# Kernel optimization log

Measured on AMD Instinct MI355X. Metric: run time of the kernel, lower is better.

## Reference

```python
import jax, jax.numpy as jnp
import numpy as np

B, S, D, H, DK, L, DFF, V = 64, 128, 512, 8, 64, 6, 2048, 72
AH = 2          # heads of the internal mask-generating attention encoder (hard-coded n_heads=2)
PRECET = 0.2    # fraction of lowest-attention prefix tokens to mask
NEG = -1e9


def pos_enc(s, d):
    pos = jnp.arange(s, dtype=jnp.float32)[:, None]
    div = jnp.exp(jnp.arange(0, d, 2, dtype=jnp.float32) * (-np.log(10000.0) / d))
    pe = jnp.zeros((s, d), jnp.float32)
    pe = pe.at[:, 0::2].set(jnp.sin(pos * div))
    pe = pe.at[:, 1::2].set(jnp.cos(pos * div))
    return pe


def ln(x, eps=1e-5):  # LayerNorm with default (identity) affine params, as in the source
    m = x.mean(-1, keepdims=True)
    v = ((x - m) ** 2).mean(-1, keepdims=True)
    return (x - m) / jnp.sqrt(v + eps)


def attn_block(x, pad, WQ, WK, WV, WO, heads):
    b, s, _ = x.shape
    dk = WQ.shape[1] // heads
    q = (x @ WQ).reshape(b, s, heads, dk).transpose(0, 2, 1, 3)
    k = (x @ WK).reshape(b, s, heads, dk).transpose(0, 2, 1, 3)
    v = (x @ WV).reshape(b, s, heads, dk).transpose(0, 2, 1, 3)
    scores = jnp.einsum('bhqd,bhkd->bhqk', q, k) / np.sqrt(dk)
    scores = jnp.where(pad[:, None, None, :], NEG, scores)
    attn = jax.nn.softmax(scores, axis=-1)
    ascore = attn.sum(axis=2)                                   # [b, h, s] column sums
    ctx = jnp.einsum('bhqk,bhkd->bqhd', attn, v).reshape(b, s, heads * dk)
    return ln(ctx @ WO + x), attn, ascore


def ffn_block(x, W1, W2):
    return ln(jax.nn.relu(x @ W1) @ W2 + x)


def encode(x, pad, tWQ, tWK, tWV, tFC, tF1, tF2):
    def step(h, p):
        WQ, WK, WV, WO, W1, W2 = p
        h, _, asc = attn_block(h, pad, WQ, WK, WV, WO, H)
        h = ffn_block(h, W1, W2)
        return h, asc.sum(axis=1)                               # sum over heads -> [b, s]
    h, scores = jax.lax.scan(step, x, (tWQ, tWK, tWV, tFC, tF1, tF2))
    return h, scores                                            # scores: [L, b, s]


def creat_mask(col, tokens):
    # col[i, j] == 0 exactly iff token j is pad (softmax of -1e9 underflows to 0).
    b, s = tokens.shape
    iszero = col == 0.0
    has = iszero.any(axis=1)
    j0 = jnp.where(has, jnp.argmax(iszero, axis=1), s)          # first pad position
    kk = jnp.where(has, jnp.ceil(PRECET * j0.astype(jnp.float32)).astype(jnp.int32), 0)
    idx = jnp.arange(s)
    vals = jnp.where(idx[None, :] < j0[:, None], col, jnp.inf)
    ranks = jnp.argsort(jnp.argsort(vals, axis=1), axis=1)      # rank 0 = smallest attention
    keep = (ranks >= kk[:, None]).astype(tokens.dtype)
    return tokens * keep


def pre_head(x, pW1, pb1, pW2, pb2, pW3, pb3):
    x = jax.nn.relu(x @ pW1 + pb1)
    x = jax.nn.relu(x @ pW2 + pb2)
    return x @ pW3 + pb3


def setup_inputs():
    key = jax.random.key(0)
    ks = jax.random.split(key, 18)
    g = lambda k, shp: jax.random.normal(k, shp, jnp.float32) * 0.02
    return {
        'tokens': jax.random.randint(ks[0], (B, S), 0, V, dtype=jnp.int32),
        'emb': g(ks[1], (V, D)),
        'aWQ': g(ks[2], (D, AH * DK)), 'aWK': g(ks[3], (D, AH * DK)), 'aWV': g(ks[4], (D, AH * DK)),
        'aFC': g(ks[5], (AH * DK, D)), 'aF1': g(ks[6], (D, DFF)), 'aF2': g(ks[7], (DFF, D)),
        'tWQ': g(ks[8], (L, D, H * DK)), 'tWK': g(ks[9], (L, D, H * DK)), 'tWV': g(ks[10], (L, D, H * DK)),
        'tFC': g(ks[11], (L, H * DK, D)), 'tF1': g(ks[12], (L, D, DFF)), 'tF2': g(ks[13], (L, DFF, D)),
        'pW1': g(ks[14], (D * S, 1024)), 'pb1': jnp.zeros((1024,), jnp.float32),
        'pW2': g(ks[15], (1024, 512)), 'pb2': jnp.zeros((512,), jnp.float32),
        'pW3': g(ks[16], (512, 128)), 'pb3': jnp.zeros((128,), jnp.float32),
    }


def reference(tokens, emb, aWQ, aWK, aWV, aFC, aF1, aF2,
              tWQ, tWK, tWV, tFC, tF1, tF2,
              pW1, pb1, pW2, pb2, pW3, pb3):
    pe = pos_enc(S, D)[None]
    pad = tokens == 0
    x = emb[tokens] + pe
    # 1-layer / 2-head mask-generating encoder; only its attn matrix is consumed downstream
    _, mattn, _ = attn_block(x, pad, aWQ, aWK, aWV, aFC, AH)
    col = mattn.sum(axis=1).sum(axis=1)                         # heads then queries -> [B, S]
    mtok = creat_mask(col, tokens)
    xm = emb[mtok] + pe
    h, scores = encode(x, pad, tWQ, tWK, tWV, tFC, tF1, tF2)
    hm, _ = encode(xm, mtok == 0, tWQ, tWK, tWV, tFC, tF1, tF2)
    out1 = pre_head(h.reshape(B, -1), pW1, pb1, pW2, pb2, pW3, pb3)
    outm = pre_head(hm.reshape(B, -1), pW1, pb1, pW2, pb2, pW3, pb3)
    return tokens, out1, mtok, outm, scores
```

## Files before the change

kernel.cpp:

```cpp
#include <hip/hip_runtime.h>
#include <hip/hip_bf16.h>
#include <math.h>

using u16 = unsigned short;
using u32 = unsigned int;

constexpr int B   = 64;
constexpr int S   = 128;
constexpr int D   = 512;
constexpr int H   = 8;
constexpr int DK  = 64;
constexpr int L   = 6;
constexpr int DFF = 2048;
constexpr int AH  = 2;
constexpr int BS  = B * S;
constexpr int BS2 = 2 * BS;

constexpr long OUT_TOK    = 0;
constexpr long OUT_OUT1   = 8192;
constexpr long OUT_MTOK   = 16384;
constexpr long OUT_OUTM   = 24576;
constexpr long OUT_SCORES = 32768;

constexpr long OFF_PE   = 0;
constexpr long OFF_ASC  = 65536;
constexpr long OFF_COLP = 196608;
constexpr long OFF_MTOK = 212992;
constexpr long OFF_X    = 221184;
constexpr long OFF_XB   = 8609792;
constexpr long OFF_QB   = 12804096;
constexpr long OFF_KB   = 16998400;
constexpr long OFF_VB   = 21192704;
constexpr long OFF_TB   = 25387008;
constexpr long OFF_W    = 42164224;
constexpr long WSTRIDE  = 3145728;

typedef __attribute__((ext_vector_type(8))) short bf16x8;
typedef __attribute__((ext_vector_type(4))) float f32x4;

__device__ __forceinline__ float b2f(u16 u) {
    union { u32 i; float f; } v; v.i = ((u32)u) << 16; return v.f;
}
__device__ __forceinline__ u16 f2b(float f) {
    union { float f; u32 i; } v; v.f = f;
    u32 r = v.i + 0x7fffu + ((v.i >> 16) & 1u);
    return (u16)(r >> 16);
}

#define GLOAD_LDS16(g, l) __builtin_amdgcn_global_load_lds(                        \
    (const __attribute__((address_space(1))) u32*)(const void*)(g),               \
    (__attribute__((address_space(3))) u32*)(void*)(l), 16, 0, 0)

__global__ void pe_kernel(float* __restrict__ pe) {
    int idx = blockIdx.x * 256 + threadIdx.x;
    if (idx >= S * (D / 2)) return;
    int s = idx >> 8;
    int i = idx & 255;
    const float CPE = (float)(-9.210340371976184 / 512.0);
    float div = expf((float)(2 * i) * CPE);
    float ang = (float)s * div;
    pe[(long)s * D + 2 * i]     = sinf(ang);
    pe[(long)s * D + 2 * i + 1] = cosf(ang);
}

__global__ void embed_dual(const int* __restrict__ toks, const float* __restrict__ emb,
                           const float* __restrict__ pe, float* __restrict__ x,
                           u16* __restrict__ xb) {
    int i8 = blockIdx.x * 256 + threadIdx.x;
    if (i8 >= BS * D / 8) return;
    int row = i8 >> 6;
    int c8  = i8 & 63;
    int s   = row & (S - 1);
    int t   = toks[row];
    float4 e0 = *(const float4*)(emb + (long)t * D + c8 * 8);
    float4 e1 = *(const float4*)(emb + (long)t * D + c8 * 8 + 4);
    float4 p0 = *(const float4*)(pe + (long)s * D + c8 * 8);
    float4 p1 = *(const float4*)(pe + (long)s * D + c8 * 8 + 4);
    float4 o0, o1;
    o0.x = e0.x + p0.x; o0.y = e0.y + p0.y; o0.z = e0.z + p0.z; o0.w = e0.w + p0.w;
    o1.x = e1.x + p1.x; o1.y = e1.y + p1.y; o1.z = e1.z + p1.z; o1.w = e1.w + p1.w;
    *(float4*)(x + (long)i8 * 8)     = o0;
    *(float4*)(x + (long)i8 * 8 + 4) = o1;
    u16 u[8] = {f2b(o0.x), f2b(o0.y), f2b(o0.z), f2b(o0.w), f2b(o1.x), f2b(o1.y), f2b(o1.z), f2b(o1.w)};
    *(uint4*)(xb + (long)i8 * 8) = *(uint4*)u;
}

__global__ __launch_bounds__(256)
void wconv_all(const float* __restrict__ tWQ, const float* __restrict__ tWK,
               const float* __restrict__ tWV, const float* __restrict__ tFC,
               const float* __restrict__ tF1, const float* __restrict__ tF2,
               u16* __restrict__ wAll) {
    __shared__ float t[32][33];
    const int lyr = blockIdx.x / 3072;
    const int bid = blockIdx.x % 3072;
    u16* base = wAll + (long)lyr * WSTRIDE;
    const float* src; u16* dst; int KK, NN, tk, tn;
    if (bid < 1024) {
        int which = bid >> 8, tt = bid & 255;
        src = (which == 0 ? tWQ : which == 1 ? tWK : which == 2 ? tWV : tFC) + (long)lyr * D * D;
        dst = base + (long)which * 262144;
        KK = 512; NN = 512; tk = tt >> 4; tn = tt & 15;
    } else if (bid < 2048) {
        int tt = bid - 1024;
        src = tF1 + (long)lyr * D * DFF; dst = base + 1048576;
        KK = 512; NN = 2048; tk = tt >> 6; tn = tt & 63;
    } else {
        int tt = bid - 2048;
        src = tF2 + (long)lyr * DFF * D; dst = base + 2097152;
        KK = 2048; NN = 512; tk = tt >> 4; tn = tt & 15;
    }
    int ty = threadIdx.x >> 5, tx = threadIdx.x & 31;
    #pragma unroll
    for (int i = 0; i < 4; i++)
        t[ty + i * 8][tx] = src[(long)(tk * 32 + ty + i * 8) * NN + tn * 32 + tx];
    __syncthreads();
    #pragma unroll
    for (int i = 0; i < 4; i++)
        dst[(long)(tn * 32 + ty + i * 8) * KK + tk * 32 + tx] = f2b(t[tx][ty + i * 8]);
}

template<int EPI, int OUTB>
__device__ __forceinline__ void gemm_core(
        const u16* __restrict__ A, const u16* __restrict__ Wt,
        float* C, u16* Cb, const float* __restrict__ X,
        int M, int N, int K, int m0, int n0) {
    __shared__ u16 As[128 * 32];
    __shared__ u16 Bs[128 * 32];
    const int tid = threadIdx.x;
    const int w = tid >> 6, l = tid & 63;
    const int wr = (w >> 1) * 64, wc = (w & 1) * 64;
    f32x4 acc[4][4];
    #pragma unroll
    for (int i = 0; i < 4; i++)
        #pragma unroll
        for (int j = 0; j < 4; j++) { f32x4 z = {0.f, 0.f, 0.f, 0.f}; acc[i][j] = z; }

    const int srow = w * 32 + (l >> 2);
    const int scol = (l & 3) * 8;
    const u16* gA = A + (long)(m0 + srow) * K + scol;
    const u16* gB = Wt + (long)(n0 + srow) * K + scol;
    u16* lA0 = As + w * 1024;
    u16* lA1 = As + w * 1024 + 512;
    u16* lB0 = Bs + w * 1024;
    u16* lB1 = Bs + w * 1024 + 512;

    for (int k0 = 0; k0 < K; k0 += 32) {
        GLOAD_LDS16(gA + k0,               lA0);
        GLOAD_LDS16(gA + (long)16 * K + k0, lA1);
        GLOAD_LDS16(gB + k0,               lB0);
        GLOAD_LDS16(gB + (long)16 * K + k0, lB1);
        __syncthreads();
        bf16x8 aF[4], bF[4];
        #pragma unroll
        for (int mi = 0; mi < 4; mi++)
            aF[mi] = *(const bf16x8*)(As + (wr + mi * 16 + (l & 15)) * 32 + (l >> 4) * 8);
        #pragma unroll
        for (int ni = 0; ni < 4; ni++)
            bF[ni] = *(const bf16x8*)(Bs + (wc + ni * 16 + (l & 15)) * 32 + (l >> 4) * 8);
        #pragma unroll
        for (int mi = 0; mi < 4; mi++)
            #pragma unroll
            for (int ni = 0; ni < 4; ni++)
                acc[mi][ni] = __builtin_amdgcn_mfma_f32_16x16x32_bf16(aF[mi], bF[ni], acc[mi][ni], 0, 0, 0);
        __syncthreads();
    }

    #pragma unroll
    for (int mi = 0; mi < 4; mi++) {
        #pragma unroll
        for (int ni = 0; ni < 4; ni++) {
            const int col = n0 + wc + ni * 16 + (l & 15);
            #pragma unroll
            for (int r = 0; r < 4; r++) {
                const int row = m0 + wr + mi * 16 + (l >> 4) * 4 + r;
                const long idx = (long)row * N + col;
                float v = acc[mi][ni][r];
                if (EPI == 1) v += X[idx];
                if (EPI == 2) v = fmaxf(v, 0.0f);
                if (OUTB) Cb[idx] = f2b(v);
                else      C[idx]  = v;
            }
        }
    }
}

__global__ __launch_bounds__(256)
void gemm_qkv_b(const u16* __restrict__ A, const u16* wq, const u16* wk, const u16* wv,
                u16* qb, u16* kb, u16* vb, int M, int N, int K) {
    const u16* Wt = blockIdx.z == 0 ? wq : blockIdx.z == 1 ? wk : wv;
    u16* Cb       = blockIdx.z == 0 ? qb : blockIdx.z == 1 ? kb : vb;
    gemm_core<0, 1>(A, Wt, nullptr, Cb, nullptr, M, N, K, blockIdx.x * 128, blockIdx.y * 128);
}
__global__ __launch_bounds__(256)
void gemm_resid_b(const u16* __restrict__ A, const u16* __restrict__ Wt,
                  float* C, const float* __restrict__ X, int M, int N, int K) {
    gemm_core<1, 0>(A, Wt, C, nullptr, X, M, N, K, blockIdx.x * 128, blockIdx.y * 128);
}
__global__ __launch_bounds__(256)
void gemm_relu_b(const u16* __restrict__ A, const u16* __restrict__ Wt,
                 u16* Cb, int M, int N, int K) {
    gemm_core<2, 1>(A, Wt, nullptr, Cb, nullptr, M, N, K, blockIdx.x * 128, blockIdx.y * 128);
}

template<int EPI>
__global__ __launch_bounds__(256)
void gemm64(const float* __restrict__ A, const float* __restrict__ W,
            float* C, const float* X, int M, int N, int K) {
    __shared__ float As[32][68];
    __shared__ float Ws[32][64];
    const int m0 = blockIdx.x * 64, n0 = blockIdx.y * 64;
    const int tid  = threadIdx.x;
    const int tr   = tid >> 4, tc = tid & 15;
    const int arow = tid >> 3, acg = tid & 7;
    const int wrow = tid >> 4, wcg = tid & 15;
    float acc[4][4] = {};
    for (int k0 = 0; k0 < K; k0 += 32) {
        float4 a0 = *(const float4*)(A + (long)(m0 + arow) * K + k0 + acg * 4);
        float4 a1 = *(const float4*)(A + (long)(m0 + arow + 32) * K + k0 + acg * 4);
        float4 w0 = *(const float4*)(W + (long)(k0 + wrow) * N + n0 + wcg * 4);
        float4 w1 = *(const float4*)(W + (long)(k0 + wrow + 16) * N + n0 + wcg * 4);
        As[acg * 4 + 0][arow] = a0.x; As[acg * 4 + 1][arow] = a0.y;
        As[acg * 4 + 2][arow] = a0.z; As[acg * 4 + 3][arow] = a0.w;
        As[acg * 4 + 0][arow + 32] = a1.x; As[acg * 4 + 1][arow + 32] = a1.y;
        As[acg * 4 + 2][arow + 32] = a1.z; As[acg * 4 + 3][arow + 32] = a1.w;
        *(float4*)&Ws[wrow][wcg * 4]      = w0;
        *(float4*)&Ws[wrow + 16][wcg * 4] = w1;
        __syncthreads();
        #pragma unroll
        for (int kk = 0; kk < 32; kk++) {
            float4 av = *(const float4*)&As[kk][tr * 4];
            float4 bv = *(const float4*)&Ws[kk][tc * 4];
            acc[0][0] += av.x * bv.x; acc[0][1] += av.x * bv.y; acc[0][2] += av.x * bv.z; acc[0][3] += av.x * bv.w;
            acc[1][0] += av.y * bv.x; acc[1][1] += av.y * bv.y; acc[1][2] += av.y * bv.z; acc[1][3] += av.y * bv.w;
            acc[2][0] += av.z * bv.x; acc[2][1] += av.z * bv.y; acc[2][2] += av.z * bv.z; acc[2][3] += av.z * bv.w;
            acc[3][0] += av.w * bv.x; acc[3][1] += av.w * bv.y; acc[3][2] += av.w * bv.z; acc[3][3] += av.w * bv.w;
        }
        __syncthreads();
    }
    #pragma unroll
    for (int i = 0; i < 4; i++) {
        int row = m0 + tr * 4 + i;
        #pragma unroll
        for (int j = 0; j < 4; j++) {
            int col = n0 + tc * 4 + j;
            long idx = (long)row * N + col;
            float v = acc[i][j];
            if (EPI == 1) v += X[idx];
            if (EPI == 3 || EPI == 4) v += X[col];
            if (EPI == 2 || EPI == 4) v = fmaxf(v, 0.0f);
            C[idx] = v;
        }
    }
}

__global__ __launch_bounds__(256)
void gemm64_qkv(const float* __restrict__ A,
                const float* __restrict__ WQ, const float* __restrict__ WK, const float* __restrict__ WV,
                float* q, float* k, float* v, int M, int N, int K) {
    __shared__ float As[32][68];
    __shared__ float Ws[32][64];
    const float* W = (blockIdx.z == 0) ? WQ : (blockIdx.z == 1) ? WK : WV;
    float*       C = (blockIdx.z == 0) ? q  : (blockIdx.z == 1) ? k  : v;
    const int m0 = blockIdx.x * 64, n0 = blockIdx.y * 64;
    const int tid  = threadIdx.x;
    const int tr   = tid >> 4, tc = tid & 15;
    const int arow = tid >> 3, acg = tid & 7;
    const int wrow = tid >> 4, wcg = tid & 15;
    float acc[4][4] = {};
    for (int k0 = 0; k0 < K; k0 += 32) {
        float4 a0 = *(const float4*)(A + (long)(m0 + arow) * K + k0 + acg * 4);
        float4 a1 = *(const float4*)(A + (long)(m0 + arow + 32) * K + k0 + acg * 4);
        float4 w0 = *(const float4*)(W + (long)(k0 + wrow) * N + n0 + wcg * 4);
        float4 w1 = *(const float4*)(W + (long)(k0 + wrow + 16) * N + n0 + wcg * 4);
        As[acg * 4 + 0][arow] = a0.x; As[acg * 4 + 1][arow] = a0.y;
        As[acg * 4 + 2][arow] = a0.z; As[acg * 4 + 3][arow] = a0.w;
        As[acg * 4 + 0][arow + 32] = a1.x; As[acg * 4 + 1][arow + 32] = a1.y;
        As[acg * 4 + 2][arow + 32] = a1.z; As[acg * 4 + 3][arow + 32] = a1.w;
        *(float4*)&Ws[wrow][wcg * 4]      = w0;
        *(float4*)&Ws[wrow + 16][wcg * 4] = w1;
        __syncthreads();
        #pragma unroll
        for (int kk = 0; kk < 32; kk++) {
            float4 av = *(const float4*)&As[kk][tr * 4];
            float4 bv = *(const float4*)&Ws[kk][tc * 4];
            acc[0][0] += av.x * bv.x; acc[0][1] += av.x * bv.y; acc[0][2] += av.x * bv.z; acc[0][3] += av.x * bv.w;
            acc[1][0] += av.y * bv.x; acc[1][1] += av.y * bv.y; acc[1][2] += av.y * bv.z; acc[1][3] += av.y * bv.w;
            acc[2][0] += av.z * bv.x; acc[2][1] += av.z * bv.y; acc[2][2] += av.z * bv.z; acc[2][3] += av.z * bv.w;
            acc[3][0] += av.w * bv.x; acc[3][1] += av.w * bv.y; acc[3][2] += av.w * bv.z; acc[3][3] += av.w * bv.w;
        }
        __syncthreads();
    }
    #pragma unroll
    for (int i = 0; i < 4; i++)
        #pragma unroll
        for (int j = 0; j < 4; j++)
            C[(long)(m0 + tr * 4 + i) * N + n0 + tc * 4 + j] = acc[i][j];
}

__global__ __launch_bounds__(256)
void gemm_ph1(const u16* __restrict__ Ah, const u16* __restrict__ Ahm,
              const float* __restrict__ W, float* __restrict__ P, int KC) {
    constexpr int N = 1024, K = 65536;
    __shared__ u16 As[128 * 32];
    __shared__ u16 Bs[128 * 32];
    const int n0 = blockIdx.x * 128;
    const int kbeg = blockIdx.y * KC;
    const int tid = threadIdx.x;
    const int w = tid >> 6, l = tid & 63;
    const int wr = w * 32;
    const int nl = tid >> 1, seg = tid & 1;
    const u16* aptr = (nl < 64 ? Ah + (long)nl * K : Ahm + (long)(nl - 64) * K) + seg * 16;
    const float* wcol = W + n0 + nl;

    f32x4 acc[2][8];
    #pragma unroll
    for (int mi = 0; mi < 2; mi++)
        #pragma unroll
        for (int ni = 0; ni < 8; ni++) { f32x4 z = {0.f, 0.f, 0.f, 0.f}; acc[mi][ni] = z; }

    for (int ks = 0; ks < KC; ks += 32) {
        const int k0 = kbeg + ks;
        uint4 a0 = *(const uint4*)(aptr + k0);
        uint4 a1 = *(const uint4*)(aptr + k0 + 8);
        float wv[16];
        #pragma unroll
        for (int j = 0; j < 16; j++)
            wv[j] = wcol[(long)(k0 + seg * 16 + j) * N];
        __syncthreads();
        *(uint4*)(As + nl * 32 + seg * 16)     = a0;
        *(uint4*)(As + nl * 32 + seg * 16 + 8) = a1;
        u32 pk[8];
        #pragma unroll
        for (int j = 0; j < 8; j++)
            pk[j] = (u32)f2b(wv[2 * j]) | ((u32)f2b(wv[2 * j + 1]) << 16);
        *(uint4*)(Bs + nl * 32 + seg * 16)     = *(uint4*)&pk[0];
        *(uint4*)(Bs + nl * 32 + seg * 16 + 8) = *(uint4*)&pk[4];
        __syncthreads();
        bf16x8 aF0 = *(const bf16x8*)(As + (wr + (l & 15)) * 32 + (l >> 4) * 8);
        bf16x8 aF1 = *(const bf16x8*)(As + (wr + 16 + (l & 15)) * 32 + (l >> 4) * 8);
        #pragma unroll
        for (int ni = 0; ni < 8; ni++) {
            bf16x8 bF = *(const bf16x8*)(Bs + (ni * 16 + (l & 15)) * 32 + (l >> 4) * 8);
            acc[0][ni] = __builtin_amdgcn_mfma_f32_16x16x32_bf16(aF0, bF, acc[0][ni], 0, 0, 0);
            acc[1][ni] = __builtin_amdgcn_mfma_f32_16x16x32_bf16(aF1, bF, acc[1][ni], 0, 0, 0);
        }
    }
    float* Pz = P + (long)blockIdx.y * 128 * N;
    #pragma unroll
    for (int mi = 0; mi < 2; mi++)
        #pragma unroll
        for (int ni = 0; ni < 8; ni++) {
            const int col = n0 + ni * 16 + (l & 15);
            #pragma unroll
            for (int r = 0; r < 4; r++)
                Pz[(long)(wr + mi * 16 + (l >> 4) * 4 + r) * N + col] = acc[mi][ni][r];
        }
}

__global__ __launch_bounds__(128)
void attn_kernel(const float* __restrict__ Q, const float* __restrict__ K,
                 const int* __restrict__ toks, float* __restrict__ colsum, int Hn) {
    __shared__ float sc[S][129];
    __shared__ float KV[S][DK];
    __shared__ int   padS[S];
    const int b = blockIdx.x / Hn;
    const int h = blockIdx.x % Hn;
    const int stride = Hn * DK;
    const int tid = threadIdx.x;

    for (int idx = tid; idx < S * DK; idx += 128) {
        int r = idx >> 6, c = idx & 63;
        KV[r][c] = K[(long)(b * S + r) * stride + h * DK + c];
    }
    padS[tid] = (toks[b * S + tid] == 0) ? 1 : 0;
    float qreg[DK];
    {
        const float* qp = Q + (long)(b * S + tid) * stride + h * DK;
        #pragma unroll
        for (int i = 0; i < 16; i++) {
            float4 t4 = *(const float4*)(qp + i * 4);
            qreg[i * 4 + 0] = t4.x; qreg[i * 4 + 1] = t4.y;
            qreg[i * 4 + 2] = t4.z; qreg[i * 4 + 3] = t4.w;
        }
    }
    __syncthreads();
    for (int k = 0; k < S; k++) {
        float s = 0.0f;
        #pragma unroll
        for (int d4 = 0; d4 < 16; d4++) {
            float4 kv = *(const float4*)&KV[k][d4 * 4];
            s += qreg[d4 * 4 + 0] * kv.x + qreg[d4 * 4 + 1] * kv.y
               + qreg[d4 * 4 + 2] * kv.z + qreg[d4 * 4 + 3] * kv.w;
        }
        sc[tid][k] = padS[k] ? -1e9f : (s * 0.125f);
    }
    float mx = -INFINITY;
    for (int k = 0; k < S; k++) mx = fmaxf(mx, sc[tid][k]);
    float sum = 0.0f;
    for (int k = 0; k < S; k++) { float e = expf(sc[tid][k] - mx); sc[tid][k] = e; sum += e; }
    for (int k = 0; k < S; k++) sc[tid][k] = sc[tid][k] / sum;
    __syncthreads();
    {
        double a = 0.0;
        for (int q2 = 0; q2 < S; q2++) a += (double)sc[q2][tid];
        colsum[(long)(b * Hn + h) * S + tid] = (float)a;
    }
}

__global__ __launch_bounds__(256)
void attn_mfma_kernel(u16* qb, const u16* __restrict__ kb, const u16* __restrict__ vb,
                      const int* __restrict__ toks, const int* __restrict__ mtok,
                      float* __restrict__ colsum) {
    __shared__ u16 pool[18432];
    __shared__ u16 Vt[64 * 136];
    __shared__ float colsLds[4][128];
    __shared__ u32 padF[128];
    u16* Qs = pool;
    u16* Ks = pool + 9216;
    u16* Ps = pool;

    const int gb = blockIdx.x >> 3, h = blockIdx.x & 7;
    const int tid = threadIdx.x;
    const int w = tid >> 6, l = tid & 63;
    const long base = (long)gb * S * D + h * 64;
    const int* tsrc = (gb < B) ? (toks + (long)gb * S) : (mtok + (long)(gb - B) * S);

    for (int j = tid; j < 1024; j += 256) {
        int r = j >> 3, c = j & 7;
        uint4 uq = *(const uint4*)(qb + base + (long)r * D + c * 8);
        uint4 uk = *(const uint4*)(kb + base + (long)r * D + c * 8);
        uint4 uv = *(const uint4*)(vb + base + (long)r * D + c * 8);
        *(uint4*)(Qs + r * 72 + c * 8) = uq;
        *(uint4*)(Ks + r * 72 + c * 8) = uk;
        u16 vv[8]; *(uint4*)vv = uv;
        #pragma unroll
        for (int t = 0; t < 8; t++) Vt[(c * 8 + t) * 136 + r] = vv[t];
    }
    if (tid < 128) padF[tid] = (tsrc[tid] == 0) ? 1u : 0u;
    __syncthreads();

    const int rowB = w * 32;
    f32x4 acc[2][8];
    #pragma unroll
    for (int mi = 0; mi < 2; mi++)
        #pragma unroll
        for (int ni = 0; ni < 8; ni++) { f32x4 z = {0.f, 0.f, 0.f, 0.f}; acc[mi][ni] = z; }
    #pragma unroll
    for (int ks = 0; ks < 2; ks++) {
        bf16x8 a0 = *(const bf16x8*)(Qs + (rowB + (l & 15)) * 72 + ks * 32 + (l >> 4) * 8);
        bf16x8 a1 = *(const bf16x8*)(Qs + (rowB + 16 + (l & 15)) * 72 + ks * 32 + (l >> 4) * 8);
        #pragma unroll
        for (int ni = 0; ni < 8; ni++) {
            bf16x8 bv = *(const bf16x8*)(Ks + (ni * 16 + (l & 15)) * 72 + ks * 32 + (l >> 4) * 8);
            acc[0][ni] = __builtin_amdgcn_mfma_f32_16x16x32_bf16(a0, bv, acc[0][ni], 0, 0, 0);
            acc[1][ni] = __builtin_amdgcn_mfma_f32_16x16x32_bf16(a1, bv, acc[1][ni], 0, 0, 0);
        }
    }
    float pf[8];
    #pragma unroll
    for (int ni = 0; ni < 8; ni++) pf[ni] = padF[ni * 16 + (l & 15)] ? 1.0f : 0.0f;
    #pragma unroll
    for (int mi = 0; mi < 2; mi++)
        #pragma unroll
        for (int ni = 0; ni < 8; ni++)
            #pragma unroll
            for (int r = 0; r < 4; r++) {
                float v = acc[mi][ni][r] * 0.125f;
                acc[mi][ni][r] = (pf[ni] != 0.0f) ? -1e9f : v;
            }
    #pragma unroll
    for (int mi = 0; mi < 2; mi++)
        #pragma unroll
        for (int r = 0; r < 4; r++) {
            float m = -INFINITY;
            #pragma unroll
            for (int ni = 0; ni < 8; ni++) m = fmaxf(m, acc[mi][ni][r]);
            m = fmaxf(m, __shfl_xor(m, 1)); m = fmaxf(m, __shfl_xor(m, 2));
            m = fmaxf(m, __shfl_xor(m, 4)); m = fmaxf(m, __shfl_xor(m, 8));
            float s = 0.0f;
            #pragma unroll
            for (int ni = 0; ni < 8; ni++) { float e = expf(acc[mi][ni][r] - m); acc[mi][ni][r] = e; s += e; }
            s += __shfl_xor(s, 1); s += __shfl_xor(s, 2);
            s += __shfl_xor(s, 4); s += __shfl_xor(s, 8);
            float inv = 1.0f / s;
            #pragma unroll
            for (int ni = 0; ni < 8; ni++) acc[mi][ni][r] *= inv;
        }
    float cs[8];
    #pragma unroll
    for (int ni = 0; ni < 8; ni++) {
        float s = 0.0f;
        #pragma unroll
        for (int mi = 0; mi < 2; mi++)
            #pragma unroll
            for (int r = 0; r < 4; r++) s += acc[mi][ni][r];
        s += __shfl_xor(s, 16); s += __shfl_xor(s, 32);
        cs[ni] = s;
    }
    __syncthreads();
    if (l < 16)
        #pragma unroll
        for (int ni = 0; ni < 8; ni++) colsLds[w][ni * 16 + l] = cs[ni];
    #pragma unroll
    for (int mi = 0; mi < 2; mi++)
        #pragma unroll
        for (int ni = 0; ni < 8; ni++)
            #pragma unroll
            for (int r = 0; r < 4; r++)
                Ps[(rowB + mi * 16 + (l >> 4) * 4 + r) * 136 + ni * 16 + (l & 15)] =
                    f2b(acc[mi][ni][r]);
    __syncthreads();
    if (tid < 128) {
        float s = colsLds[0][tid] + colsLds[1][tid] + colsLds[2][tid] + colsLds[3][tid];
        colsum[((long)gb * H + h) * S + tid] = s;
    }
    f32x4 o[2][4];
    #pragma unroll
    for (int mi = 0; mi < 2; mi++)
        #pragma unroll
        for (int n = 0; n < 4; n++) { f32x4 z = {0.f, 0.f, 0.f, 0.f}; o[mi][n] = z; }
    #pragma unroll
    for (int ks = 0; ks < 4; ks++) {
        bf16x8 p0 = *(const bf16x8*)(Ps + (rowB + (l & 15)) * 136 + ks * 32 + (l >> 4) * 8);
        bf16x8 p1 = *(const bf16x8*)(Ps + (rowB + 16 + (l & 15)) * 136 + ks * 32 + (l >> 4) * 8);
        #pragma unroll
        for (int n = 0; n < 4; n++) {
            bf16x8 bv = *(const bf16x8*)(Vt + (n * 16 + (l & 15)) * 136 + ks * 32 + (l >> 4) * 8);
            o[0][n] = __builtin_amdgcn_mfma_f32_16x16x32_bf16(p0, bv, o[0][n], 0, 0, 0);
            o[1][n] = __builtin_amdgcn_mfma_f32_16x16x32_bf16(p1, bv, o[1][n], 0, 0, 0);
        }
    }
    #pragma unroll
    for (int mi = 0; mi < 2; mi++)
        #pragma unroll
        for (int n = 0; n < 4; n++) {
            const int col = n * 16 + (l & 15);
            #pragma unroll
            for (int r = 0; r < 4; r++) {
                const int row = rowB + mi * 16 + (l >> 4) * 4 + r;
                qb[base + (long)row * D + col] = f2b(o[mi][n][r]);
            }
        }
}

__global__ __launch_bounds__(128)
void creat_mask_kernel(const float* __restrict__ colpart, const int* __restrict__ toks,
                       int* __restrict__ mtok, float* __restrict__ out) {
    __shared__ float colS[S];
    __shared__ int   j0s, kks;
    const int b = blockIdx.x, j = threadIdx.x;
    float c = colpart[(long)(b * AH + 0) * S + j] + colpart[(long)(b * AH + 1) * S + j];
    colS[j] = c;
    int tk = toks[b * S + j];
    __syncthreads();
    if (j == 0) {
        int j0 = S;
        for (int i = 0; i < S; i++) if (colS[i] == 0.0f) { j0 = i; break; }
        int kk = (j0 < S) ? (int)ceilf(0.2f * (float)j0) : 0;
        j0s = j0; kks = kk;
    }
    __syncthreads();
    const int j0 = j0s, kk = kks;
    float vj = (j < j0) ? colS[j] : INFINITY;
    int rank = 0;
    for (int i = 0; i < S; i++) {
        float vi = (i < j0) ? colS[i] : INFINITY;
        if (vi < vj || (vi == vj && i < j)) rank++;
    }
    int mt = (rank >= kk) ? tk : 0;
    mtok[b * S + j] = mt;
    out[OUT_TOK + b * S + j]  = (float)tk;
    out[OUT_MTOK + b * S + j] = (float)mt;
}

__global__ __launch_bounds__(256)
void ln_kernel(float* __restrict__ x, u16* __restrict__ xb) {
    const int row  = blockIdx.x * 4 + (threadIdx.x >> 6);
    const int lane = threadIdx.x & 63;
    float* r = x + (long)row * D;
    float4 v0 = *(const float4*)(r + lane * 4);
    float4 v1 = *(const float4*)(r + 256 + lane * 4);
    float s = v0.x + v0.y + v0.z + v0.w + v1.x + v1.y + v1.z + v1.w;
    #pragma unroll
    for (int off = 32; off; off >>= 1) s += __shfl_xor(s, off);
    float m = s * (1.0f / 512.0f);
    float d0 = v0.x - m, d1 = v0.y - m, d2 = v0.z - m, d3 = v0.w - m;
    float d4 = v1.x - m, d5 = v1.y - m, d6 = v1.z - m, d7 = v1.w - m;
    float q = d0*d0 + d1*d1 + d2*d2 + d3*d3 + d4*d4 + d5*d5 + d6*d6 + d7*d7;
    #pragma unroll
    for (int off = 32; off; off >>= 1) q += __shfl_xor(q, off);
    float inv = 1.0f / sqrtf(q * (1.0f / 512.0f) + 1e-5f);
    float4 o0, o1;
    o0.x = d0 * inv; o0.y = d1 * inv; o0.z = d2 * inv; o0.w = d3 * inv;
    o1.x = d4 * inv; o1.y = d5 * inv; o1.z = d6 * inv; o1.w = d7 * inv;
    *(float4*)(r + lane * 4)       = o0;
    *(float4*)(r + 256 + lane * 4) = o1;
    u16* rb = xb + (long)row * D;
    u16 p0[4] = {f2b(o0.x), f2b(o0.y), f2b(o0.z), f2b(o0.w)};
    u16 p1[4] = {f2b(o1.x), f2b(o1.y), f2b(o1.z), f2b(o1.w)};
    *(uint2*)(rb + lane * 4)       = *(uint2*)p0;
    *(uint2*)(rb + 256 + lane * 4) = *(uint2*)p1;
}

__global__ void score_reduce_kernel(const float* __restrict__ ascorep, float* __restrict__ dst) {
    int idx = blockIdx.x * 256 + threadIdx.x;
    if (idx >= B * S) return;
    int b = idx >> 7, j = idx & 127;
    float s = 0.0f;
    for (int h = 0; h < H; h++) s += ascorep[(long)(b * H + h) * S + j];
    dst[idx] = s;
}

__global__ void reduce1_kernel(const float* __restrict__ parts, const float* __restrict__ b1,
                               float* __restrict__ o) {
    int idx = blockIdx.x * 256 + threadIdx.x;
    if (idx >= 128 * 1024) return;
    float s = 0.0f;
    for (int z = 0; z < 64; z++) s += parts[(long)z * 128 * 1024 + idx];
    s += b1[idx & 1023];
    o[idx] = fmaxf(s, 0.0f);
}

__global__ void pack_out_kernel(const float* __restrict__ ph3, float* __restrict__ out) {
    int idx = blockIdx.x * 256 + threadIdx.x;
    if (idx >= 128 * 128) return;
    int row = idx >> 7, col = idx & 127;
    long base = (row < 64) ? (OUT_OUT1 + (long)row * 128) : (OUT_OUTM + (long)(row - 64) * 128);
    out[base + col] = ph3[idx];
}

extern "C" void kernel_launch(void* const* d_in, const int* in_sizes, int n_in,
                              void* d_out, int out_size, void* d_ws, size_t ws_size,
                              hipStream_t stream) {
    const int*   toks = (const int*)d_in[0];
    const float* emb  = (const float*)d_in[1];
    const float* aWQ  = (const float*)d_in[2];
    const float* aWK  = (const float*)d_in[3];
    const float* tWQ  = (const float*)d_in[8];
    const float* tWK  = (const float*)d_in[9];
    const float* tWV  = (const float*)d_in[10];
    const float* tFC  = (const float*)d_in[11];
    const float* tF1  = (const float*)d_in[12];
    const float* tF2  = (const float*)d_in[13];
    const float* pW1  = (const float*)d_in[14];
    const float* pb1  = (const float*)d_in[15];
    const float* pW2  = (const float*)d_in[16];
    const float* pb2  = (const float*)d_in[17];
    const float* pW3  = (const float*)d_in[18];
    const float* pb3  = (const float*)d_in[19];
    float* out = (float*)d_out;

    float* ws   = (float*)d_ws;
    float* pe   = ws + OFF_PE;
    float* ascp = ws + OFF_ASC;
    float* colp = ws + OFF_COLP;
    int*   mtok = (int*)(ws + OFF_MTOK);
    float* x    = ws + OFF_X;
    u16*   xb   = (u16*)(ws + OFF_XB);
    u16*   qb   = (u16*)(ws + OFF_QB);
    u16*   kb   = (u16*)(ws + OFF_KB);
    u16*   vb   = (u16*)(ws + OFF_VB);
    u16*   tb   = (u16*)(ws + OFF_TB);
    u16*   wAll = (u16*)(ws + OFF_W);

    float* maq   = ws + OFF_TB;
    float* mak   = maq + (long)BS * 128;
    float* parts = ws + OFF_TB;
    float* ph1o  = parts + 8388608;
    float* ph2o  = ph1o + 131072;
    float* ph3o  = ph2o + 65536;

    pe_kernel<<<128, 256, 0, stream>>>(pe);
    wconv_all<<<6 * 3072, 256, 0, stream>>>(tWQ, tWK, tWV, tFC, tF1, tF2, wAll);
    embed_dual<<<2048, 256, 0, stream>>>(toks, emb, pe, x, xb);

    gemm64_qkv<<<dim3(BS / 64, 2, 2), 256, 0, stream>>>(
        x, aWQ, aWK, nullptr, maq, mak, nullptr, BS, AH * DK, D);
    attn_kernel<<<B * AH, 128, 0, stream>>>(maq, mak, toks, colp, AH);
    creat_mask_kernel<<<B, 128, 0, stream>>>(colp, toks, mtok, out);
    embed_dual<<<2048, 256, 0, stream>>>(mtok, emb, pe, x + (long)BS * D, xb + (long)BS * D);

    for (int l = 0; l < L; l++) {
        const u16* wq = wAll + (long)l * WSTRIDE;
        const u16* wk = wq + 262144;
        const u16* wv = wq + 524288;
        const u16* wo = wq + 786432;
        const u16* w1 = wq + 1048576;
        const u16* w2 = wq + 2097152;
        gemm_qkv_b<<<dim3(BS2 / 128, D / 128, 3), 256, 0, stream>>>(
            xb, wq, wk, wv, qb, kb, vb, BS2, D, D);
        attn_mfma_kernel<<<2 * B * H, 256, 0, stream>>>(qb, kb, vb, toks, mtok, ascp);
        score_reduce_kernel<<<32, 256, 0, stream>>>(ascp, out + OUT_SCORES + (long)l * BS);
        gemm_resid_b<<<dim3(BS2 / 128, D / 128), 256, 0, stream>>>(qb, wo, x, x, BS2, D, D);
        ln_kernel<<<BS2 / 4, 256, 0, stream>>>(x, xb);
        gemm_relu_b<<<dim3(BS2 / 128, DFF / 128), 256, 0, stream>>>(xb, w1, tb, BS2, DFF, D);
        gemm_resid_b<<<dim3(BS2 / 128, D / 128), 256, 0, stream>>>(tb, w2, x, x, BS2, D, DFF);
        ln_kernel<<<BS2 / 4, 256, 0, stream>>>(x, xb);
    }

    gemm_ph1<<<dim3(8, 64), 256, 0, stream>>>(xb, xb + (long)BS * D, pW1, parts, 1024);
    reduce1_kernel<<<512, 256, 0, stream>>>(parts, pb1, ph1o);
    gemm64<4><<<dim3(2, 8), 256, 0, stream>>>(ph1o, pW2, ph2o, pb2, 128, 512, 1024);
    gemm64<3><<<dim3(2, 2), 256, 0, stream>>>(ph2o, pW3, ph3o, pb3, 128, 128, 512);
    pack_out_kernel<<<64, 256, 0, stream>>>(ph3o, out);
}
```

Before: 1.686 ms.

## Fuse residual add and LayerNorm into full-row output-projection and FFN2 GEMMs

Replaces the residual GEMM plus separate LayerNorm kernel with one GEMM whose 64-row block covers all 512 output columns, so row statistics are reduced in-block through shared memory and the normalized fp32 and bf16 activations are written directly. This removes two LN launches per layer and a full read/write pass over the fp32 activations. In exchange each block loads the whole 512-column weight slice per k-step and the grid drops to 256 blocks of 512 threads, which may lower occupancy. Variance is now computed as E[x^2]-mean^2, which is slightly less numerically stable.

```diff
diff --git a/kernel.cpp b/kernel.cpp
--- a/kernel.cpp
+++ b/kernel.cpp
@@ -192,14 +192,100 @@
     gemm_core<0, 1>(A, Wt, nullptr, Cb, nullptr, M, N, K, blockIdx.x * 128, blockIdx.y * 128);
 }
 __global__ __launch_bounds__(256)
-void gemm_resid_b(const u16* __restrict__ A, const u16* __restrict__ Wt,
-                  float* C, const float* __restrict__ X, int M, int N, int K) {
-    gemm_core<1, 0>(A, Wt, C, nullptr, X, M, N, K, blockIdx.x * 128, blockIdx.y * 128);
-}
-__global__ __launch_bounds__(256)
 void gemm_relu_b(const u16* __restrict__ A, const u16* __restrict__ Wt,
                  u16* Cb, int M, int N, int K) {
     gemm_core<2, 1>(A, Wt, nullptr, Cb, nullptr, M, N, K, blockIdx.x * 128, blockIdx.y * 128);
+}
+
+__global__ __launch_bounds__(512)
+void gemm_ln(const u16* __restrict__ A, const u16* __restrict__ Wt,
+             float* x, u16* __restrict__ xb, int K) {
+    __shared__ u16 As[64 * 32];
+    __shared__ u16 Bs[512 * 32];
+    __shared__ float redS[64][9];
+    __shared__ float redQ[64][9];
+    __shared__ float meanS[64], invS[64];
+    const int m0 = blockIdx.x * 64;
+    const int tid = threadIdx.x;
+    const int w = tid >> 6, l = tid & 63;
+    const int wc = w * 64;
+
+    f32x4 acc[4][4];
+    #pragma unroll
+    for (int i = 0; i < 4; i++)
+        #pragma unroll
+        for (int j = 0; j < 4; j++) { f32x4 z = {0.f, 0.f, 0.f, 0.f}; acc[i][j] = z; }
+
+    const int scol = (l & 3) * 8;
+    const u16* gA = A + (long)(m0 + w * 16 + (l >> 2)) * K + scol;
+    const u16* gB = Wt + (long)(w * 64 + (l >> 2)) * K + scol;
+    u16* lA = As + (w * 16) * 32;
+    u16* lB = Bs + (w * 64) * 32;
+
+    for (int k0 = 0; k0 < K; k0 += 32) {
+        if (w < 4) GLOAD_LDS16(gA + k0, lA);
+        #pragma unroll
+        for (int j = 0; j < 4; j++)
+            GLOAD_LDS16(gB + (long)j * 16 * K + k0, lB + j * 16 * 32);
+        __syncthreads();
+        bf16x8 aF[4], bF[4];
+        #pragma unroll
+        for (int mi = 0; mi < 4; mi++)
+            aF[mi] = *(const bf16x8*)(As + (mi * 16 + (l & 15)) * 32 + (l >> 4) * 8);
+        #pragma unroll
+        for (int ni = 0; ni < 4; ni++)
+            bF[ni] = *(const bf16x8*)(Bs + (wc + ni * 16 + (l & 15)) * 32 + (l >> 4) * 8);
+        #pragma unroll
+        for (int mi = 0; mi < 4; mi++)
+            #pragma unroll
+            for (int ni = 0; ni < 4; ni++)
+                acc[mi][ni] = __builtin_amdgcn_mfma_f32_16x16x32_bf16(aF[mi], bF[ni], acc[mi][ni], 0, 0, 0);
+        __syncthreads();
+    }
+
+    #pragma unroll
+    for (int mi = 0; mi < 4; mi++)
+        #pragma unroll
+        for (int r = 0; r < 4; r++) {
+            const int row = mi * 16 + (l >> 4) * 4 + r;
+            float s = 0.0f, q = 0.0f;
+            #pragma unroll
+            for (int ni = 0; ni < 4; ni++) {
+                const int col = wc + ni * 16 + (l & 15);
+                float v = acc[mi][ni][r] + x[(long)(m0 + row) * D + col];
+                acc[mi][ni][r] = v;
+                s += v; q += v * v;
+            }
+            s += __shfl_xor(s, 1); s += __shfl_xor(s, 2); s += __shfl_xor(s, 4); s += __shfl_xor(s, 8);
+            q += __shfl_xor(q, 1); q += __shfl_xor(q, 2); q += __shfl_xor(q, 4); q += __shfl_xor(q, 8);
+            if ((l & 15) == 0) { redS[row][w] = s; redQ[row][w] = q; }
+        }
+    __syncthreads();
+    if (tid < 64) {
+        float s = 0.0f, q = 0.0f;
+        #pragma unroll
+        for (int ww = 0; ww < 8; ww++) { s += redS[tid][ww]; q += redQ[tid][ww]; }
+        float mean = s * (1.0f / 512.0f);
+        float var  = q * (1.0f / 512.0f) - mean * mean;
+        meanS[tid] = mean;
+        invS[tid]  = 1.0f / sqrtf(var + 1e-5f);
+    }
+    __syncthreads();
+    #pragma unroll
+    for (int mi = 0; mi < 4; mi++)
+        #pragma unroll
+        for (int r = 0; r < 4; r++) {
+            const int row = mi * 16 + (l >> 4) * 4 + r;
+            const float mn = meanS[row], iv = invS[row];
+            #pragma unroll
+            for (int ni = 0; ni < 4; ni++) {
+                const int col = wc + ni * 16 + (l & 15);
+                const long idx = (long)(m0 + row) * D + col;
+                float o = (acc[mi][ni][r] - mn) * iv;
+                x[idx]  = o;
+                xb[idx] = f2b(o);
+            }
+        }
 }
 
 template<int EPI>
@@ -573,35 +659,6 @@
     out[OUT_MTOK + b * S + j] = (float)mt;
 }
 
-__global__ __launch_bounds__(256)
-void ln_kernel(float* __restrict__ x, u16* __restrict__ xb) {
-    const int row  = blockIdx.x * 4 + (threadIdx.x >> 6);
-    const int lane = threadIdx.x & 63;
-    float* r = x + (long)row * D;
-    float4 v0 = *(const float4*)(r + lane * 4);
-    float4 v1 = *(const float4*)(r + 256 + lane * 4);
-    float s = v0.x + v0.y + v0.z + v0.w + v1.x + v1.y + v1.z + v1.w;
-    #pragma unroll
-    for (int off = 32; off; off >>= 1) s += __shfl_xor(s, off);
-    float m = s * (1.0f / 512.0f);
-    float d0 = v0.x - m, d1 = v0.y - m, d2 = v0.z - m, d3 = v0.w - m;
-    float d4 = v1.x - m, d5 = v1.y - m, d6 = v1.z - m, d7 = v1.w - m;
-    float q = d0*d0 + d1*d1 + d2*d2 + d3*d3 + d4*d4 + d5*d5 + d6*d6 + d7*d7;
-    #pragma unroll
-    for (int off = 32; off; off >>= 1) q += __shfl_xor(q, off);
-    float inv = 1.0f / sqrtf(q * (1.0f / 512.0f) + 1e-5f);
-    float4 o0, o1;
-    o0.x = d0 * inv; o0.y = d1 * inv; o0.z = d2 * inv; o0.w = d3 * inv;
-    o1.x = d4 * inv; o1.y = d5 * inv; o1.z = d6 * inv; o1.w = d7 * inv;
-    *(float4*)(r + lane * 4)       = o0;
-    *(float4*)(r + 256 + lane * 4) = o1;
-    u16* rb = xb + (long)row * D;
-    u16 p0[4] = {f2b(o0.x), f2b(o0.y), f2b(o0.z), f2b(o0.w)};
-    u16 p1[4] = {f2b(o1.x), f2b(o1.y), f2b(o1.z), f2b(o1.w)};
-    *(uint2*)(rb + lane * 4)       = *(uint2*)p0;
-    *(uint2*)(rb + 256 + lane * 4) = *(uint2*)p1;
-}
-
 __global__ void score_reduce_kernel(const float* __restrict__ ascorep, float* __restrict__ dst) {
     int idx = blockIdx.x * 256 + threadIdx.x;
     if (idx >= B * S) return;
@@ -691,11 +748,9 @@
             xb, wq, wk, wv, qb, kb, vb, BS2, D, D);
         attn_mfma_kernel<<<2 * B * H, 256, 0, stream>>>(qb, kb, vb, toks, mtok, ascp);
         score_reduce_kernel<<<32, 256, 0, stream>>>(ascp, out + OUT_SCORES + (long)l * BS);
-        gemm_resid_b<<<dim3(BS2 / 128, D / 128), 256, 0, stream>>>(qb, wo, x, x, BS2, D, D);
-        ln_kernel<<<BS2 / 4, 256, 0, stream>>>(x, xb);
+        gemm_ln<<<BS2 / 64, 512, 0, stream>>>(qb, wo, x, xb, D);
         gemm_relu_b<<<dim3(BS2 / 128, DFF / 128), 256, 0, stream>>>(xb, w1, tb, BS2, DFF, D);
-        gemm_resid_b<<<dim3(BS2 / 128, D / 128), 256, 0, stream>>>(tb, w2, x, x, BS2, D, DFF);
-        ln_kernel<<<BS2 / 4, 256, 0, stream>>>(x, xb);
+        gemm_ln<<<BS2 / 64, 512, 0, stream>>>(tb, w2, x, xb, DFF);
     }
 
     gemm_ph1<<<dim3(8, 64), 256, 0, stream>>>(xb, xb + (long)BS * D, pW1, parts, 1024);
```

After: 1.809 ms. 1.07x slower.
